# Kernel optimization log

Measured on AMD Instinct MI355X. Metric: run time of the kernel, lower is better.

Reference implementation:

```python
import jax, jax.numpy as jnp
import numpy as np

B, N, K = 4, 40960, 16
D_IN, D_OUT = 32, 64


def setup_inputs() -> dict:
    key = jax.random.key(0)
    keys = iter(jax.random.split(key, 48))
    def nrm(shape, scale):
        return (jax.random.normal(next(keys), shape, jnp.float32) * scale).astype(jnp.float32)
    inp = {
        "feature": jax.random.normal(next(keys), (B, N, D_IN), jnp.float32),
        "xyz": jax.random.uniform(next(keys), (B, N, 3), jnp.float32),
        "neigh_idx": jax.random.randint(next(keys), (B, N, K), 0, N, jnp.int32),
    }
    def conv_bn(name, cin, cout):
        inp["w_" + name] = nrm((cin, cout), (2.0 / cin) ** 0.5)
        inp["s_" + name] = 1.0 + nrm((cout,), 0.1)  # folded BN scale: gamma/sqrt(var+eps)
        inp["b_" + name] = nrm((cout,), 0.1)        # folded BN bias: beta - mean*scale
    conv_bn("mlp1", D_IN, D_OUT // 2)
    conv_bn("lfa1", 10, D_OUT // 2)
    inp["w_att1_fc"] = nrm((D_OUT, D_OUT), (2.0 / D_OUT) ** 0.5)
    conv_bn("att1_mlp", D_OUT, D_OUT // 2)
    conv_bn("lfa2", D_OUT // 2, D_OUT // 2)
    inp["w_att2_fc"] = nrm((D_OUT, D_OUT), (2.0 / D_OUT) ** 0.5)
    conv_bn("att2_mlp", D_OUT, D_OUT)
    conv_bn("mlp2", D_OUT, 2 * D_OUT)
    conv_bn("sc", D_IN, 2 * D_OUT)
    return inp


def _gather(pc, idx):
    # pc: [B,N,D], idx: [B,N,K] -> [B,N,K,D]
    b, n, k = idx.shape
    flat = jnp.take_along_axis(pc, idx.reshape(b, n * k, 1), axis=1)
    return flat.reshape(b, n, k, pc.shape[-1])


def _cb(x, w, s, b, relu=True):
    # 1x1 conv + folded BN (+ ReLU), channels-last
    y = jnp.einsum('...i,io->...o', x, w) * s + b
    return jnp.maximum(y, 0.0) if relu else y


def _att_pool(fs, w_fc, w, s, b):
    # fs: [B,N,K,C]; softmax-attention pooling over K, then mlp
    scores = jax.nn.softmax(jnp.einsum('bnkc,cd->bnkd', fs, w_fc), axis=2)
    agg = jnp.sum(fs * scores, axis=2)  # [B,N,C]
    return _cb(agg, w, s, b)


def _rel_pos(xyz, idx):
    nbr = _gather(xyz, idx)                           # [B,N,K,3]
    tile = jnp.broadcast_to(xyz[:, :, None, :], nbr.shape)
    rel = tile - nbr
    dist = jnp.sqrt(jnp.sum(rel * rel, axis=-1, keepdims=True))
    return jnp.concatenate([dist, rel, tile, nbr], axis=-1)  # [B,N,K,10]


def reference(feature, xyz, neigh_idx,
              w_mlp1, s_mlp1, b_mlp1,
              w_lfa1, s_lfa1, b_lfa1,
              w_att1_fc, w_att1_mlp, s_att1_mlp, b_att1_mlp,
              w_lfa2, s_lfa2, b_lfa2,
              w_att2_fc, w_att2_mlp, s_att2_mlp, b_att2_mlp,
              w_mlp2, s_mlp2, b_mlp2,
              w_sc, s_sc, b_sc):
    f_pc = _cb(feature, w_mlp1, s_mlp1, b_mlp1)                   # [B,N,d/2]
    f_xyz = _cb(_rel_pos(xyz, neigh_idx), w_lfa1, s_lfa1, b_lfa1)  # [B,N,K,d/2]
    f_nb = _gather(f_pc, neigh_idx)                                # [B,N,K,d/2]
    f_agg = _att_pool(jnp.concatenate([f_nb, f_xyz], axis=-1),
                      w_att1_fc, w_att1_mlp, s_att1_mlp, b_att1_mlp)  # [B,N,d/2]
    f_xyz2 = _cb(f_xyz, w_lfa2, s_lfa2, b_lfa2)                    # [B,N,K,d/2]
    f_nb2 = _gather(f_agg, neigh_idx)                              # [B,N,K,d/2]
    f_pc2 = _att_pool(jnp.concatenate([f_nb2, f_xyz2], axis=-1),
                      w_att2_fc, w_att2_mlp, s_att2_mlp, b_att2_mlp)  # [B,N,d]
    out = _cb(f_pc2, w_mlp2, s_mlp2, b_mlp2, relu=False)           # [B,N,2d]
    sc = _cb(feature, w_sc, s_sc, b_sc, relu=False)
    return jax.nn.leaky_relu(out + sc, negative_slope=0.2)
```

## Files before the change

### kernel.cpp

```cpp
#include <hip/hip_runtime.h>
#include <hip/hip_bf16.h>

#define NPTS  40960
#define BNPTS 163840
#define KNB   16

using bf16x8 = __attribute__((ext_vector_type(8))) short;
using f32x4  = __attribute__((ext_vector_type(4))) float;

__device__ __forceinline__ unsigned short f2bf(float x) {
    union { float f; unsigned u; } v; v.f = x;
    unsigned r = v.u + 0x7fffu + ((v.u >> 16) & 1u);
    return (unsigned short)(r >> 16);
}
__device__ __forceinline__ float bf2f(unsigned short u) {
    union { unsigned u; float f; } v; v.u = ((unsigned)u) << 16;
    return v.f;
}
__device__ __forceinline__ unsigned pk2(float lo, float hi) {
    union { __hip_bfloat162 h; unsigned u; } v;
    v.h = __float22bfloat162_rn(float2{lo, hi});
    return v.u;
}
__device__ __forceinline__ bf16x8 pack8(float a0, float a1, float a2, float a3,
                                        float a4, float a5, float a6, float a7) {
    union { unsigned u[4]; bf16x8 v; } w;
    w.u[0] = pk2(a0, a1); w.u[1] = pk2(a2, a3);
    w.u[2] = pk2(a4, a5); w.u[3] = pk2(a6, a7);
    return w.v;
}
__device__ __forceinline__ f32x4 mfma16(bf16x8 a, bf16x8 b, f32x4 c) {
    return __builtin_amdgcn_mfma_f32_16x16x32_bf16(a, b, c, 0, 0, 0);
}

__global__ __launch_bounds__(256)
void k_mlp1(const float* __restrict__ feature, const float* __restrict__ w,
            const float* __restrict__ s, const float* __restrict__ b,
            unsigned short* __restrict__ f_pc)
{
    __shared__ unsigned short wT[32 * 40];
    __shared__ float sS[32], sB[32];
    const int tid = threadIdx.x;
    for (int t = tid; t < 1024; t += 256) {
        int c = t >> 5, d = t & 31;
        wT[d * 40 + c] = f2bf(w[t]);
    }
    if (tid < 32) { sS[tid] = s[tid]; sB[tid] = b[tid]; }
    __syncthreads();
    const int lid = tid & 63, wv = tid >> 6;
    const int col = lid & 15, quad = lid >> 4;
    bf16x8 B0 = *(const bf16x8*)&wT[col * 40 + quad * 8];
    bf16x8 B1 = *(const bf16x8*)&wT[(16 + col) * 40 + quad * 8];
    float s0 = sS[col], b0 = sB[col], s1 = sS[16 + col], b1 = sB[16 + col];
    for (int itp = 0; itp < 4; itp++) {
        const int p0 = blockIdx.x * 256 + wv * 64 + itp * 16;
        const float* fr = &feature[(size_t)(p0 + col) * 32 + quad * 8];
        float4 u0 = *(const float4*)fr;
        float4 u1 = *(const float4*)(fr + 4);
        bf16x8 a = pack8(u0.x, u0.y, u0.z, u0.w, u1.x, u1.y, u1.z, u1.w);
        f32x4 z = {0.f, 0.f, 0.f, 0.f};
        f32x4 d0 = mfma16(a, B0, z);
        f32x4 d1 = mfma16(a, B1, z);
        #pragma unroll
        for (int r = 0; r < 4; r++) {
            int p = p0 + quad * 4 + r;
            f_pc[(size_t)p * 32 + col]      = f2bf(fmaxf(d0[r] * s0 + b0, 0.f));
            f_pc[(size_t)p * 32 + 16 + col] = f2bf(fmaxf(d1[r] * s1 + b1, 0.f));
        }
    }
}

template<int NOUT, bool HAS_LFA2>
__global__ __launch_bounds__(256, 4)
void k_att(const float* __restrict__ xyz, const int* __restrict__ nidx,
           const unsigned short* __restrict__ src,
           const float* __restrict__ wlfa1, const float* __restrict__ slfa1, const float* __restrict__ blfa1,
           const float* __restrict__ wlfa2, const float* __restrict__ slfa2, const float* __restrict__ blfa2,
           const float* __restrict__ wfc,
           const float* __restrict__ wmlp, const float* __restrict__ smlp, const float* __restrict__ bmlp,
           unsigned short* __restrict__ out)
{
    constexpr int NP = NOUT / 32;
    constexpr int WS = 88;
    constexpr int WFCT_B = 64 * WS * 2;
    constexpr int WMT_B  = NOUT * WS * 2;
    constexpr int U_SIZE = 16384;
    __shared__ __align__(16) char smem[WFCT_B + WMT_B + U_SIZE];
    unsigned short* wfcT = (unsigned short*)smem;
    unsigned short* wmT  = (unsigned short*)(smem + WFCT_B);
    char* uni = smem + WFCT_B + WMT_B;
    unsigned short* wl1T = (unsigned short*)(uni);
    unsigned short* wl2T = (unsigned short*)(uni + 2560);
    float* sl1 = (float*)(uni + 5120);
    float* bl1 = sl1 + 32;
    float* sl2 = sl1 + 64;
    float* bl2 = sl1 + 96;
    float* sml = (float*)(uni + 5632);
    float* bml = sml + NOUT;

    const int tid = threadIdx.x;
    for (int t = tid; t < 64 * 64; t += 256) {
        int c = t >> 6, d = t & 63;
        wfcT[d * WS + c] = f2bf(wfc[t]);
    }
    for (int t = tid; t < 32 * 32; t += 256) {
        int k = t >> 5, d = t & 31;
        int slot = (d & 1) * 16 + (d >> 1);
        wl1T[slot * 40 + k] = f2bf(k < 10 ? wlfa1[k * 32 + d] : 0.f);
        if (HAS_LFA2) wl2T[slot * 40 + k] = f2bf(wlfa2[k * 32 + d]);
    }
    for (int t = tid; t < 64 * NOUT; t += 256) {
        int c = t / NOUT, d = t % NOUT;
        int slot = (d >> 5) * 32 + (d & 1) * 16 + ((d & 31) >> 1);
        wmT[slot * WS + c] = f2bf(wmlp[t]);
    }
    if (tid < 32) {
        sl1[tid] = slfa1[tid]; bl1[tid] = blfa1[tid];
        if (HAS_LFA2) { sl2[tid] = slfa2[tid]; bl2[tid] = blfa2[tid]; }
    }
    if (tid < NOUT) { sml[tid] = smlp[tid]; bml[tid] = bmlp[tid]; }
    __syncthreads();

    const int lid = tid & 63, wv = tid >> 6;
    const int col = lid & 15, quad = lid >> 4;

    bf16x8 Bl1e = *(const bf16x8*)&wl1T[col * 40 + quad * 8];
    bf16x8 Bl1o = *(const bf16x8*)&wl1T[(16 + col) * 40 + quad * 8];
    bf16x8 Bl2e{}, Bl2o{};
    if (HAS_LFA2) {
        Bl2e = *(const bf16x8*)&wl2T[col * 40 + quad * 8];
        Bl2o = *(const bf16x8*)&wl2T[(16 + col) * 40 + quad * 8];
    }
    const float sl1e = sl1[2 * col], bl1e = bl1[2 * col], sl1o = sl1[2 * col + 1], bl1o = bl1[2 * col + 1];
    float sl2e = 0.f, bl2e = 0.f, sl2o = 0.f, bl2o = 0.f;
    if (HAS_LFA2) { sl2e = sl2[2 * col]; bl2e = bl2[2 * col]; sl2o = sl2[2 * col + 1]; bl2o = bl2[2 * col + 1]; }
    float sme[NP], bme[NP], smo[NP], bmo[NP];
    #pragma unroll
    for (int tp = 0; tp < NP; tp++) {
        sme[tp] = sml[tp * 32 + 2 * col]; bme[tp] = bml[tp * 32 + 2 * col];
        smo[tp] = sml[tp * 32 + 2 * col + 1]; bmo[tp] = bml[tp * 32 + 2 * col + 1];
    }
    __syncthreads();

    unsigned short* fc  = (unsigned short*)(uni) + wv * (16 * WS);
    unsigned short* ag  = (unsigned short*)(uni + 11264) + wv * (4 * 72);
    unsigned short* nb  = (unsigned short*)(uni + 13568) + wv * 256;
    float*          cxy = (float*)(uni + 15616) + wv * 48;

    const int blk = (int)blockIdx.x;
    const int vblk = (blk & 7) * 320 + (blk >> 3);
    const int pbase = vblk * 64 + wv * 16;
    const int pb = (pbase / NPTS) * NPTS;
    const unsigned short* srcb = src + (size_t)pb * 32;
    const float* xyzb = xyz + (size_t)pb * 3;

    {
        int4 t4 = *(const int4*)&nidx[(size_t)pbase * KNB + lid * 4];
        ushort4 u = make_ushort4((unsigned short)t4.x, (unsigned short)t4.y,
                                 (unsigned short)t4.z, (unsigned short)t4.w);
        *(ushort4*)&nb[lid * 4] = u;
        if (lid < 48) cxy[lid] = xyz[(size_t)pbase * 3 + lid];
    }

    const f32x4 z = {0.f, 0.f, 0.f, 0.f};
    bf16x8 vs; float nx = 0.f, ny = 0.f, nz = 0.f;
    {
        int j = (int)nb[col];
        vs = *(const bf16x8*)(srcb + (size_t)j * 32 + quad * 8);
        if (quad < 2) { const float* xp = xyzb + (size_t)j * 3; nx = xp[0]; ny = xp[1]; nz = xp[2]; }
    }

    #pragma unroll 1
    for (int it = 0; it < 16; it++) {
        const int p = pbase + it;
        bf16x8 a0 = vs;
        *(bf16x8*)&fc[col * WS + quad * 8] = a0;

        float cx = cxy[it * 3], cy = cxy[it * 3 + 1], cz = cxy[it * 3 + 2];
        float rx = cx - nx, ry = cy - ny, rz = cz - nz;
        float dd = sqrtf(rx * rx + ry * ry + rz * rz);
        float f0 = 0.f, f1 = 0.f, f2 = 0.f, f3 = 0.f, f4 = 0.f, f5 = 0.f, f6 = 0.f, f7 = 0.f;
        if (quad == 0)      { f0 = dd; f1 = rx; f2 = ry; f3 = rz; f4 = cx; f5 = cy; f6 = cz; f7 = nx; }
        else if (quad == 1) { f0 = ny; f1 = nz; }
        bf16x8 al = pack8(f0, f1, f2, f3, f4, f5, f6, f7);

        {
            int itn = it < 15 ? it + 1 : 15;
            int j = (int)nb[itn * 16 + col];
            vs = *(const bf16x8*)(srcb + (size_t)j * 32 + quad * 8);
            if (quad < 2) { const float* xp = xyzb + (size_t)j * 3; nx = xp[0]; ny = xp[1]; nz = xp[2]; }
        }

        {
            f32x4 d0 = mfma16(al, Bl1e, z);
            f32x4 d1 = mfma16(al, Bl1o, z);
            #pragma unroll
            for (int r = 0; r < 4; r++) {
                float ye = fmaxf(d0[r] * sl1e + bl1e, 0.f);
                float yo = fmaxf(d1[r] * sl1o + bl1o, 0.f);
                *(unsigned*)&fc[(quad * 4 + r) * WS + 32 + 2 * col] = pk2(ye, yo);
            }
            if (HAS_LFA2) {
                bf16x8 a2 = *(const bf16x8*)&fc[col * WS + 32 + quad * 8];
                f32x4 e0 = mfma16(a2, Bl2e, z);
                f32x4 e1 = mfma16(a2, Bl2o, z);
                #pragma unroll
                for (int r = 0; r < 4; r++) {
                    float ye = fmaxf(e0[r] * sl2e + bl2e, 0.f);
                    float yo = fmaxf(e1[r] * sl2o + bl2o, 0.f);
                    *(unsigned*)&fc[(quad * 4 + r) * WS + 32 + 2 * col] = pk2(ye, yo);
                }
            }
        }

        {
            bf16x8 a1 = *(const bf16x8*)&fc[col * WS + 32 + quad * 8];
            #pragma unroll
            for (int nt = 0; nt < 4; nt++) {
                bf16x8 B0 = *(const bf16x8*)&wfcT[(nt * 16 + col) * WS + quad * 8];
                bf16x8 B1 = *(const bf16x8*)&wfcT[(nt * 16 + col) * WS + 32 + quad * 8];
                f32x4 L = mfma16(a1, B1, mfma16(a0, B0, z));
                float e0 = __expf(L[0]), e1 = __expf(L[1]), e2 = __expf(L[2]), e3 = __expf(L[3]);
                float sden = (e0 + e1) + (e2 + e3);
                const unsigned short* frr = &fc[quad * 4 * WS + nt * 16 + col];
                float av = e0 * bf2f(frr[0]) + e1 * bf2f(frr[WS]) + e2 * bf2f(frr[2 * WS]) + e3 * bf2f(frr[3 * WS]);
                av   += __shfl_xor(av, 16, 64);
                sden += __shfl_xor(sden, 16, 64);
                av   += __shfl_xor(av, 32, 64);
                sden += __shfl_xor(sden, 32, 64);
                if (quad == 0) ag[(it & 3) * 72 + nt * 16 + col] = f2bf(av / sden);
            }
        }

        if ((it & 3) == 3) {
            bf16x8 am0 = *(const bf16x8*)&ag[(col & 3) * 72 + quad * 8];
            bf16x8 am1 = *(const bf16x8*)&ag[(col & 3) * 72 + 32 + quad * 8];
            #pragma unroll
            for (int tp = 0; tp < NP; tp++) {
                bf16x8 Be0 = *(const bf16x8*)&wmT[(tp * 32 + col) * WS + quad * 8];
                bf16x8 Be1 = *(const bf16x8*)&wmT[(tp * 32 + col) * WS + 32 + quad * 8];
                bf16x8 Bo0 = *(const bf16x8*)&wmT[(tp * 32 + 16 + col) * WS + quad * 8];
                bf16x8 Bo1 = *(const bf16x8*)&wmT[(tp * 32 + 16 + col) * WS + 32 + quad * 8];
                f32x4 de = mfma16(am1, Be1, mfma16(am0, Be0, z));
                f32x4 dq = mfma16(am1, Bo1, mfma16(am0, Bo0, z));
                if (quad == 0) {
                    #pragma unroll
                    for (int r = 0; r < 4; r++) {
                        float ye = fmaxf(de[r] * sme[tp] + bme[tp], 0.f);
                        float yo = fmaxf(dq[r] * smo[tp] + bmo[tp], 0.f);
                        *(unsigned*)&out[(size_t)(p - 3 + r) * NOUT + tp * 32 + 2 * col] = pk2(ye, yo);
                    }
                }
            }
        }
    }
}

__global__ __launch_bounds__(256)
void k_out(const unsigned short* __restrict__ f_pc2, const float* __restrict__ feature,
           const float* __restrict__ w2, const float* __restrict__ s2, const float* __restrict__ b2,
           const float* __restrict__ wsc, const float* __restrict__ ssc, const float* __restrict__ bsc,
           float* __restrict__ out)
{
    __shared__ unsigned short w2T[128 * 88];
    __shared__ unsigned short wsT[128 * 40];
    __shared__ float sA[128], sB2[128], sC[128];
    const int tid = threadIdx.x;
    for (int t = tid; t < 64 * 128; t += 256) {
        int c = t >> 7, d = t & 127;
        w2T[d * 88 + c] = f2bf(w2[t]);
    }
    for (int t = tid; t < 32 * 128; t += 256) {
        int c = t >> 7, d = t & 127;
        wsT[d * 40 + c] = f2bf(wsc[t]);
    }
    if (tid < 128) { sA[tid] = s2[tid]; sB2[tid] = ssc[tid]; sC[tid] = b2[tid] + bsc[tid]; }
    __syncthreads();
    const int lid = tid & 63, wv = tid >> 6;
    const int col = lid & 15, quad = lid >> 4;
    const f32x4 z = {0.f, 0.f, 0.f, 0.f};
    #pragma unroll 1
    for (int itp = 0; itp < 4; itp++) {
        const int p0 = blockIdx.x * 256 + wv * 64 + itp * 16;
        const unsigned short* ar = &f_pc2[(size_t)(p0 + col) * 64 + quad * 8];
        bf16x8 a10 = *(const bf16x8*)ar;
        bf16x8 a11 = *(const bf16x8*)(ar + 32);
        const float* fr = &feature[(size_t)(p0 + col) * 32 + quad * 8];
        float4 u0 = *(const float4*)fr;
        float4 u1 = *(const float4*)(fr + 4);
        bf16x8 a2 = pack8(u0.x, u0.y, u0.z, u0.w, u1.x, u1.y, u1.z, u1.w);
        #pragma unroll
        for (int nt = 0; nt < 8; nt++) {
            bf16x8 bk0 = *(const bf16x8*)&w2T[(nt * 16 + col) * 88 + quad * 8];
            bf16x8 bk1 = *(const bf16x8*)&w2T[(nt * 16 + col) * 88 + 32 + quad * 8];
            bf16x8 bs  = *(const bf16x8*)&wsT[(nt * 16 + col) * 40 + quad * 8];
            f32x4 d = mfma16(a11, bk1, mfma16(a10, bk0, z));
            f32x4 e = mfma16(a2, bs, z);
            int n = nt * 16 + col;
            float ss = sA[n], st = sB2[n], bb = sC[n];
            #pragma unroll
            for (int r = 0; r < 4; r++) {
                float y = d[r] * ss + e[r] * st + bb;
                y = y > 0.f ? y : 0.2f * y;
                out[(size_t)(p0 + quad * 4 + r) * 128 + n] = y;
            }
        }
    }
}

extern "C" void kernel_launch(void* const* d_in, const int* in_sizes, int n_in,
                              void* d_out, int out_size, void* d_ws, size_t ws_size,
                              hipStream_t stream) {
    const float* feature = (const float*)d_in[0];
    const float* xyz     = (const float*)d_in[1];
    const int*   nidx    = (const int*)d_in[2];
    const float* w_mlp1 = (const float*)d_in[3];
    const float* s_mlp1 = (const float*)d_in[4];
    const float* b_mlp1 = (const float*)d_in[5];
    const float* w_lfa1 = (const float*)d_in[6];
    const float* s_lfa1 = (const float*)d_in[7];
    const float* b_lfa1 = (const float*)d_in[8];
    const float* w_att1_fc  = (const float*)d_in[9];
    const float* w_att1_mlp = (const float*)d_in[10];
    const float* s_att1_mlp = (const float*)d_in[11];
    const float* b_att1_mlp = (const float*)d_in[12];
    const float* w_lfa2 = (const float*)d_in[13];
    const float* s_lfa2 = (const float*)d_in[14];
    const float* b_lfa2 = (const float*)d_in[15];
    const float* w_att2_fc  = (const float*)d_in[16];
    const float* w_att2_mlp = (const float*)d_in[17];
    const float* s_att2_mlp = (const float*)d_in[18];
    const float* b_att2_mlp = (const float*)d_in[19];
    const float* w_mlp2 = (const float*)d_in[20];
    const float* s_mlp2 = (const float*)d_in[21];
    const float* b_mlp2 = (const float*)d_in[22];
    const float* w_sc = (const float*)d_in[23];
    const float* s_sc = (const float*)d_in[24];
    const float* b_sc = (const float*)d_in[25];

    unsigned short* f_pc  = (unsigned short*)d_ws;
    unsigned short* f_agg = f_pc  + (size_t)BNPTS * 32;
    unsigned short* f_pc2 = f_agg + (size_t)BNPTS * 32;
    float* out = (float*)d_out;

    k_mlp1<<<BNPTS / 256, 256, 0, stream>>>(feature, w_mlp1, s_mlp1, b_mlp1, f_pc);
    k_att<32, false><<<BNPTS / 64, 256, 0, stream>>>(
        xyz, nidx, f_pc,
        w_lfa1, s_lfa1, b_lfa1,
        w_lfa1, s_lfa1, b_lfa1,
        w_att1_fc, w_att1_mlp, s_att1_mlp, b_att1_mlp, f_agg);
    k_att<64, true><<<BNPTS / 64, 256, 0, stream>>>(
        xyz, nidx, f_agg,
        w_lfa1, s_lfa1, b_lfa1,
        w_lfa2, s_lfa2, b_lfa2,
        w_att2_fc, w_att2_mlp, s_att2_mlp, b_att2_mlp, f_pc2);
    k_out<<<BNPTS / 256, 256, 0, stream>>>(
        f_pc2, feature,
        w_mlp2, s_mlp2, b_mlp2,
        w_sc, s_sc, b_sc, out);
}
```

Baseline: 397.2 us.

## Hold attention weights in registers, fold BN into lfa1, use fast exp2/rcp

Moves the attention FC weights, and for the 32-wide variant the MLP weights, out of shared memory into per-lane registers, shrinking LDS so more blocks fit per CU. It folds the lfa1 BN scale and bias into the weight matrix through a constant-1 input channel, and pre-scales the FC weights by log2(e) so the softmax can use hardware exp2 and reciprocal instead of expf and division. Separately, k_out now handles half as many points per block and launches twice as many blocks. The trade-off is higher register pressure and slightly less precise exp and reciprocal.

```diff
diff --git a/kernel.cpp b/kernel.cpp
--- a/kernel.cpp
+++ b/kernel.cpp
@@ -32,6 +32,8 @@
 __device__ __forceinline__ f32x4 mfma16(bf16x8 a, bf16x8 b, f32x4 c) {
     return __builtin_amdgcn_mfma_f32_16x16x32_bf16(a, b, c, 0, 0, 0);
 }
+__device__ __forceinline__ float exp2_fast(float x) { return __builtin_amdgcn_exp2f(x); }
+__device__ __forceinline__ float rcp_fast(float x)  { return __builtin_amdgcn_rcpf(x); }
 
 __global__ __launch_bounds__(256)
 void k_mlp1(const float* __restrict__ feature, const float* __restrict__ w,
@@ -82,65 +84,104 @@
 {
     constexpr int NP = NOUT / 32;
     constexpr int WS = 88;
-    constexpr int WFCT_B = 64 * WS * 2;
-    constexpr int WMT_B  = NOUT * WS * 2;
+    constexpr int WMT_B = (NOUT == 64) ? NOUT * WS * 2 : 0;
     constexpr int U_SIZE = 16384;
-    __shared__ __align__(16) char smem[WFCT_B + WMT_B + U_SIZE];
-    unsigned short* wfcT = (unsigned short*)smem;
-    unsigned short* wmT  = (unsigned short*)(smem + WFCT_B);
-    char* uni = smem + WFCT_B + WMT_B;
-    unsigned short* wl1T = (unsigned short*)(uni);
-    unsigned short* wl2T = (unsigned short*)(uni + 2560);
-    float* sl1 = (float*)(uni + 5120);
-    float* bl1 = sl1 + 32;
-    float* sl2 = sl1 + 64;
-    float* bl2 = sl1 + 96;
-    float* sml = (float*)(uni + 5632);
-    float* bml = sml + NOUT;
+    __shared__ __align__(16) char smem[WMT_B + U_SIZE];
+    unsigned short* wmT = (unsigned short*)smem;
+    char* uni = smem + WMT_B;
 
     const int tid = threadIdx.x;
-    for (int t = tid; t < 64 * 64; t += 256) {
-        int c = t >> 6, d = t & 63;
-        wfcT[d * WS + c] = f2bf(wfc[t]);
-    }
-    for (int t = tid; t < 32 * 32; t += 256) {
-        int k = t >> 5, d = t & 31;
-        int slot = (d & 1) * 16 + (d >> 1);
-        wl1T[slot * 40 + k] = f2bf(k < 10 ? wlfa1[k * 32 + d] : 0.f);
-        if (HAS_LFA2) wl2T[slot * 40 + k] = f2bf(wlfa2[k * 32 + d]);
-    }
-    for (int t = tid; t < 64 * NOUT; t += 256) {
-        int c = t / NOUT, d = t % NOUT;
-        int slot = (d >> 5) * 32 + (d & 1) * 16 + ((d & 31) >> 1);
-        wmT[slot * WS + c] = f2bf(wmlp[t]);
-    }
-    if (tid < 32) {
-        sl1[tid] = slfa1[tid]; bl1[tid] = blfa1[tid];
-        if (HAS_LFA2) { sl2[tid] = slfa2[tid]; bl2[tid] = blfa2[tid]; }
-    }
-    if (tid < NOUT) { sml[tid] = smlp[tid]; bml[tid] = bmlp[tid]; }
-    __syncthreads();
-
     const int lid = tid & 63, wv = tid >> 6;
     const int col = lid & 15, quad = lid >> 4;
 
-    bf16x8 Bl1e = *(const bf16x8*)&wl1T[col * 40 + quad * 8];
-    bf16x8 Bl1o = *(const bf16x8*)&wl1T[(16 + col) * 40 + quad * 8];
-    bf16x8 Bl2e{}, Bl2o{};
-    if (HAS_LFA2) {
-        Bl2e = *(const bf16x8*)&wl2T[col * 40 + quad * 8];
-        Bl2o = *(const bf16x8*)&wl2T[(16 + col) * 40 + quad * 8];
-    }
-    const float sl1e = sl1[2 * col], bl1e = bl1[2 * col], sl1o = sl1[2 * col + 1], bl1o = bl1[2 * col + 1];
+    {
+        unsigned short* wfcS = (unsigned short*)uni;
+        for (int t = tid; t < 64 * 64; t += 256) {
+            int c = t >> 6, d = t & 63;
+            wfcS[d * WS + c] = f2bf(wfc[t] * 1.4426950408889634f);
+        }
+        if (NOUT == 64) {
+            for (int t = tid; t < 64 * NOUT; t += 256) {
+                int c = t / NOUT, d = t % NOUT;
+                int slot = (d >> 5) * 32 + (d & 1) * 16 + ((d & 31) >> 1);
+                wmT[slot * WS + c] = f2bf(wmlp[t]);
+            }
+        }
+    }
+    __syncthreads();
+    bf16x8 Bfc[4][2];
+    {
+        const unsigned short* wfcS = (const unsigned short*)uni;
+        #pragma unroll
+        for (int nt = 0; nt < 4; nt++)
+            #pragma unroll
+            for (int ks = 0; ks < 2; ks++)
+                Bfc[nt][ks] = *(const bf16x8*)&wfcS[(nt * 16 + col) * WS + ks * 32 + quad * 8];
+    }
+    __syncthreads();
+
+    {
+        unsigned short* wl1S = (unsigned short*)uni;
+        unsigned short* wl2S = (unsigned short*)(uni + 2560);
+        float* sl2S = (float*)(uni + 5120);
+        float* bl2S = sl2S + 32;
+        float* smlS = (float*)(uni + 5632);
+        float* bmlS = smlS + NOUT;
+        for (int t = tid; t < 32 * 32; t += 256) {
+            int k = t >> 5, d = t & 31;
+            int slot = (d & 1) * 16 + (d >> 1);
+            float v1 = k < 10 ? wlfa1[k * 32 + d] * slfa1[d] : (k == 10 ? blfa1[d] : 0.f);
+            wl1S[slot * 40 + k] = f2bf(v1);
+            if (HAS_LFA2) wl2S[slot * 40 + k] = f2bf(wlfa2[k * 32 + d]);
+        }
+        if (HAS_LFA2 && tid < 32) { sl2S[tid] = slfa2[tid]; bl2S[tid] = blfa2[tid]; }
+        if (tid < NOUT) { smlS[tid] = smlp[tid]; bmlS[tid] = bmlp[tid]; }
+    }
+    __syncthreads();
+    bf16x8 Bl1e, Bl1o, Bl2e{}, Bl2o{};
     float sl2e = 0.f, bl2e = 0.f, sl2o = 0.f, bl2o = 0.f;
-    if (HAS_LFA2) { sl2e = sl2[2 * col]; bl2e = bl2[2 * col]; sl2o = sl2[2 * col + 1]; bl2o = bl2[2 * col + 1]; }
     float sme[NP], bme[NP], smo[NP], bmo[NP];
-    #pragma unroll
-    for (int tp = 0; tp < NP; tp++) {
-        sme[tp] = sml[tp * 32 + 2 * col]; bme[tp] = bml[tp * 32 + 2 * col];
-        smo[tp] = sml[tp * 32 + 2 * col + 1]; bmo[tp] = bml[tp * 32 + 2 * col + 1];
-    }
-    __syncthreads();
+    {
+        const unsigned short* wl1S = (const unsigned short*)uni;
+        const unsigned short* wl2S = (const unsigned short*)(uni + 2560);
+        const float* sl2S = (const float*)(uni + 5120);
+        const float* bl2S = sl2S + 32;
+        const float* smlS = (const float*)(uni + 5632);
+        const float* bmlS = smlS + NOUT;
+        Bl1e = *(const bf16x8*)&wl1S[col * 40 + quad * 8];
+        Bl1o = *(const bf16x8*)&wl1S[(16 + col) * 40 + quad * 8];
+        if (HAS_LFA2) {
+            Bl2e = *(const bf16x8*)&wl2S[col * 40 + quad * 8];
+            Bl2o = *(const bf16x8*)&wl2S[(16 + col) * 40 + quad * 8];
+            sl2e = sl2S[2 * col]; bl2e = bl2S[2 * col];
+            sl2o = sl2S[2 * col + 1]; bl2o = bl2S[2 * col + 1];
+        }
+        #pragma unroll
+        for (int tp = 0; tp < NP; tp++) {
+            sme[tp] = smlS[tp * 32 + 2 * col]; bme[tp] = bmlS[tp * 32 + 2 * col];
+            smo[tp] = smlS[tp * 32 + 2 * col + 1]; bmo[tp] = bmlS[tp * 32 + 2 * col + 1];
+        }
+    }
+    __syncthreads();
+
+    bf16x8 Bme_r[NP][2], Bmo_r[NP][2];
+    if constexpr (NOUT == 32) {
+        unsigned short* wmS = (unsigned short*)uni;
+        for (int t = tid; t < 64 * NOUT; t += 256) {
+            int c = t / NOUT, d = t % NOUT;
+            int slot = (d >> 5) * 32 + (d & 1) * 16 + ((d & 31) >> 1);
+            wmS[slot * WS + c] = f2bf(wmlp[t]);
+        }
+        __syncthreads();
+        #pragma unroll
+        for (int tp = 0; tp < NP; tp++)
+            #pragma unroll
+            for (int ks = 0; ks < 2; ks++) {
+                Bme_r[tp][ks] = *(const bf16x8*)&wmS[(tp * 32 + col) * WS + ks * 32 + quad * 8];
+                Bmo_r[tp][ks] = *(const bf16x8*)&wmS[(tp * 32 + 16 + col) * WS + ks * 32 + quad * 8];
+            }
+        __syncthreads();
+    }
 
     unsigned short* fc  = (unsigned short*)(uni) + wv * (16 * WS);
     unsigned short* ag  = (unsigned short*)(uni + 11264) + wv * (4 * 72);
@@ -181,7 +222,7 @@
         float dd = sqrtf(rx * rx + ry * ry + rz * rz);
         float f0 = 0.f, f1 = 0.f, f2 = 0.f, f3 = 0.f, f4 = 0.f, f5 = 0.f, f6 = 0.f, f7 = 0.f;
         if (quad == 0)      { f0 = dd; f1 = rx; f2 = ry; f3 = rz; f4 = cx; f5 = cy; f6 = cz; f7 = nx; }
-        else if (quad == 1) { f0 = ny; f1 = nz; }
+        else if (quad == 1) { f0 = ny; f1 = nz; f2 = 1.0f; }
         bf16x8 al = pack8(f0, f1, f2, f3, f4, f5, f6, f7);
 
         {
@@ -196,8 +237,8 @@
             f32x4 d1 = mfma16(al, Bl1o, z);
             #pragma unroll
             for (int r = 0; r < 4; r++) {
-                float ye = fmaxf(d0[r] * sl1e + bl1e, 0.f);
-                float yo = fmaxf(d1[r] * sl1o + bl1o, 0.f);
+                float ye = fmaxf(d0[r], 0.f);
+                float yo = fmaxf(d1[r], 0.f);
                 *(unsigned*)&fc[(quad * 4 + r) * WS + 32 + 2 * col] = pk2(ye, yo);
             }
             if (HAS_LFA2) {
@@ -217,10 +258,9 @@
             bf16x8 a1 = *(const bf16x8*)&fc[col * WS + 32 + quad * 8];
             #pragma unroll
             for (int nt = 0; nt < 4; nt++) {
-                bf16x8 B0 = *(const bf16x8*)&wfcT[(nt * 16 + col) * WS + quad * 8];
-                bf16x8 B1 = *(const bf16x8*)&wfcT[(nt * 16 + col) * WS + 32 + quad * 8];
-                f32x4 L = mfma16(a1, B1, mfma16(a0, B0, z));
-                float e0 = __expf(L[0]), e1 = __expf(L[1]), e2 = __expf(L[2]), e3 = __expf(L[3]);
+                f32x4 L = mfma16(a1, Bfc[nt][1], mfma16(a0, Bfc[nt][0], z));
+                float e0 = exp2_fast(L[0]), e1 = exp2_fast(L[1]);
+                float e2 = exp2_fast(L[2]), e3 = exp2_fast(L[3]);
                 float sden = (e0 + e1) + (e2 + e3);
                 const unsigned short* frr = &fc[quad * 4 * WS + nt * 16 + col];
                 float av = e0 * bf2f(frr[0]) + e1 * bf2f(frr[WS]) + e2 * bf2f(frr[2 * WS]) + e3 * bf2f(frr[3 * WS]);
@@ -228,7 +268,7 @@
                 sden += __shfl_xor(sden, 16, 64);
                 av   += __shfl_xor(av, 32, 64);
                 sden += __shfl_xor(sden, 32, 64);
-                if (quad == 0) ag[(it & 3) * 72 + nt * 16 + col] = f2bf(av / sden);
+                if (quad == 0) ag[(it & 3) * 72 + nt * 16 + col] = f2bf(av * rcp_fast(sden));
             }
         }
 
@@ -237,10 +277,16 @@
             bf16x8 am1 = *(const bf16x8*)&ag[(col & 3) * 72 + 32 + quad * 8];
             #pragma unroll
             for (int tp = 0; tp < NP; tp++) {
-                bf16x8 Be0 = *(const bf16x8*)&wmT[(tp * 32 + col) * WS + quad * 8];
-                bf16x8 Be1 = *(const bf16x8*)&wmT[(tp * 32 + col) * WS + 32 + quad * 8];
-                bf16x8 Bo0 = *(const bf16x8*)&wmT[(tp * 32 + 16 + col) * WS + quad * 8];
-                bf16x8 Bo1 = *(const bf16x8*)&wmT[(tp * 32 + 16 + col) * WS + 32 + quad * 8];
+                bf16x8 Be0, Be1, Bo0, Bo1;
+                if constexpr (NOUT == 32) {
+                    Be0 = Bme_r[tp][0]; Be1 = Bme_r[tp][1];
+                    Bo0 = Bmo_r[tp][0]; Bo1 = Bmo_r[tp][1];
+                } else {
+                    Be0 = *(const bf16x8*)&wmT[(tp * 32 + col) * WS + quad * 8];
+                    Be1 = *(const bf16x8*)&wmT[(tp * 32 + col) * WS + 32 + quad * 8];
+                    Bo0 = *(const bf16x8*)&wmT[(tp * 32 + 16 + col) * WS + quad * 8];
+                    Bo1 = *(const bf16x8*)&wmT[(tp * 32 + 16 + col) * WS + 32 + quad * 8];
+                }
                 f32x4 de = mfma16(am1, Be1, mfma16(am0, Be0, z));
                 f32x4 dq = mfma16(am1, Bo1, mfma16(am0, Bo0, z));
                 if (quad == 0) {
@@ -280,8 +326,8 @@
     const int col = lid & 15, quad = lid >> 4;
     const f32x4 z = {0.f, 0.f, 0.f, 0.f};
     #pragma unroll 1
-    for (int itp = 0; itp < 4; itp++) {
-        const int p0 = blockIdx.x * 256 + wv * 64 + itp * 16;
+    for (int itp = 0; itp < 2; itp++) {
+        const int p0 = blockIdx.x * 128 + wv * 32 + itp * 16;
         const unsigned short* ar = &f_pc2[(size_t)(p0 + col) * 64 + quad * 8];
         bf16x8 a10 = *(const bf16x8*)ar;
         bf16x8 a11 = *(const bf16x8*)(ar + 32);
@@ -354,7 +400,7 @@
         w_lfa1, s_lfa1, b_lfa1,
         w_lfa2, s_lfa2, b_lfa2,
         w_att2_fc, w_att2_mlp, s_att2_mlp, b_att2_mlp, f_pc2);
-    k_out<<<BNPTS / 256, 256, 0, stream>>>(
+    k_out<<<BNPTS / 128, 256, 0, stream>>>(
         f_pc2, feature,
         w_mlp2, s_mlp2, b_mlp2,
         w_sc, s_sc, b_sc, out);
```

Result: faster. 375.2 us (-5.5%).
